# Kernel optimization log

Hardware: AMD Instinct MI355X
Metric: run time of the kernel (lower is better)

The kernel has to match this reference:

```python
import jax, jax.numpy as jnp
import numpy as np

N_ATOMS = 8_000_000
N_REC = 2_000_000
N_POC = 500_000
N_CHAINS = 4


def setup_inputs() -> dict:
    key = jax.random.key(0)
    k1, k2, k3, k4 = jax.random.split(key, 4)
    # coordinates in nm, inside a ~5 nm box
    positions = jax.random.uniform(k1, (N_ATOMS, 3), dtype=jnp.float32) * 5.0
    box_vectors = jnp.diag(jnp.array([5.0, 5.0, 5.0], dtype=jnp.float32))
    # unique receptor atom indices into positions
    rec_indices = jax.random.permutation(k2, N_ATOMS)[:N_REC].astype(jnp.int32)
    # unique pocket indices INTO THE REC ARRAY (poc_pos = rec_pos[poc_indices])
    poc_indices = jax.random.permutation(k3, N_REC)[:N_POC].astype(jnp.int32)
    # contiguous chain assignment over rec atoms, all chains present in pocket
    chain_ids = ((jnp.arange(N_REC, dtype=jnp.int32) * N_CHAINS) // N_REC).astype(jnp.int32)
    poc_chain_ids = chain_ids[poc_indices]
    ref_poc = jax.random.uniform(k4, (N_POC, 3), dtype=jnp.float32) * 5.0
    k = jnp.float32(100.0)  # kJ/mol/nm^2
    return {
        "positions": positions, "box_vectors": box_vectors, "ref_poc": ref_poc,
        "k": k, "rec_indices": rec_indices, "poc_indices": poc_indices,
        "chain_ids": chain_ids, "poc_chain_ids": poc_chain_ids, "n_chains": N_CHAINS,
    }


def best_periodic_translation(pos1, pos2, box_vectors):
    # pos1, pos2: [C,3]; box_vectors: [3,3] (rows are lattice vectors)
    delta = pos2 - pos1
    inv = 1.0 / jnp.diag(box_vectors)
    s3 = jnp.round(delta[:, 2] * inv[2])
    delta = delta - s3[:, None] * box_vectors[2]
    s2 = jnp.round(delta[:, 1] * inv[1])
    delta = delta - s2[:, None] * box_vectors[1]
    s1 = jnp.round(delta[:, 0] * inv[0])
    return s1[:, None] * box_vectors[0] + s2[:, None] * box_vectors[1] + s3[:, None] * box_vectors[2]


def reference(positions, box_vectors, ref_poc, k, rec_indices, poc_indices, chain_ids, poc_chain_ids, n_chains):
    rec_pos = positions[rec_indices]  # [R,3]
    # Per-chain pocket COM. NOTE: original indexes global positions here
    # (positions[poc_chain_indices]), NOT rec_pos -- reproduced faithfully.
    poc_glob = positions[poc_indices]  # [P,3]
    counts = jax.ops.segment_sum(jnp.ones((poc_glob.shape[0],), poc_glob.dtype), poc_chain_ids, num_segments=n_chains)  # [C]
    poc_com = jax.ops.segment_sum(poc_glob, poc_chain_ids, num_segments=n_chains) / counts[:, None]  # [C,3]
    ref_com = jax.ops.segment_sum(ref_poc, poc_chain_ids, num_segments=n_chains) / counts[:, None]  # [C,3]
    best_t = best_periodic_translation(poc_com, ref_com, box_vectors)  # [C,3]
    rec_pos = rec_pos + best_t[chain_ids]  # translate each chain into the reference image

    poc_pos = rec_pos[poc_indices]  # [P,3]
    rec_origin = jnp.mean(rec_pos, axis=0)
    rec_centered = rec_pos - rec_origin
    r_sq = jnp.sum(rec_centered ** 2, axis=1)  # [R]
    F = jnp.zeros_like(rec_pos).at[poc_indices].set(-2.0 * k * (poc_pos - ref_poc))
    F_mean = jnp.mean(F, axis=0)
    torque = jnp.cross(rec_centered, F)
    torque_mean = jnp.mean(torque, axis=0)
    F_rot = jnp.cross(torque_mean[None], rec_centered) / r_sq[:, None]
    F_final = jnp.zeros_like(positions).at[rec_indices].set(F_mean + F_rot)
    return (jnp.float32(0.0), F_final)
```

## Files before the change

### kernel.cpp

```cpp
#include <hip/hip_runtime.h>


typedef unsigned int uint32;
typedef unsigned char uchar;

#define MAXC 16
#define W_BT 0
#define W_O 48
#define W_FM 52
#define W_TM 56
#define W_ACC 64

#define GCOUNT_OFF 4096
#define REC_OFF 8192
#define NB 512
#define BSH 14
#define BUCKET_ATOMS (1 << BSH)
#define CAP 5120
#define INV8_OFF (REC_OFF + NB * CAP * 4)

#define PB 512
#define RB 512
#define K1_KPT 16
#define K1_CHUNK (256 * K1_KPT)

struct PartSh { uint32 hist[NB]; uint32 curs[NB]; uint32 base[NB]; };
struct PocSh  { float red[4][43]; float accL[3 + MAXC * 10]; };
union ShU { PartSh part; PocSh poc; };

__device__ inline float waveSum(float v) {
#pragma unroll
  for (int off = 32; off > 0; off >>= 1) v += __shfl_down(v, off, 64);
  return v;
}

__global__ __launch_bounds__(256) void k_fused(
    const float* __restrict__ pos, const float* __restrict__ ref_poc,
    const int* __restrict__ rec_idx, const int* __restrict__ cid,
    const int* __restrict__ poc_idx, const int* __restrict__ poc_cid,
    const int* __restrict__ ncp, int R, int P,
    uint32* __restrict__ gcount, uint32* __restrict__ grecords,
    float* __restrict__ ws) {
  const int tid = threadIdx.x;
  const int bid = blockIdx.x;
  __shared__ ShU sh;
  const int C = ncp[0];

  if (bid < PB) {
    const int gsz = PB * 256;
    if (C <= 4) {
      float vals[43];
#pragma unroll
      for (int v = 0; v < 43; ++v) vals[v] = 0.f;
      for (int rb = bid * 256 + tid; rb < P; rb += 4 * gsz) {
        int rr[4], i2[4], c2[4], ri[4];
        float g[4][3], p[4][3], rf[4][3];
#pragma unroll
        for (int q = 0; q < 4; ++q) {
          int r = rb + q * gsz;
          rr[q] = (r < P) ? r : -1;
        }
#pragma unroll
        for (int q = 0; q < 4; ++q) {
          int r = (rr[q] < 0) ? 0 : rr[q];
          i2[q] = poc_idx[r];
          c2[q] = poc_cid[r];
        }
#pragma unroll
        for (int q = 0; q < 4; ++q) {
          ri[q] = rec_idx[i2[q]];
          g[q][0] = pos[3 * i2[q] + 0];
          g[q][1] = pos[3 * i2[q] + 1];
          g[q][2] = pos[3 * i2[q] + 2];
        }
#pragma unroll
        for (int q = 0; q < 4; ++q) {
          int r = (rr[q] < 0) ? 0 : rr[q];
          p[q][0] = pos[3 * ri[q] + 0];
          p[q][1] = pos[3 * ri[q] + 1];
          p[q][2] = pos[3 * ri[q] + 2];
          rf[q][0] = ref_poc[3 * r + 0];
          rf[q][1] = ref_poc[3 * r + 1];
          rf[q][2] = ref_poc[3 * r + 2];
        }
#pragma unroll
        for (int q = 0; q < 4; ++q) {
          if (rr[q] >= 0) {
            vals[0] += p[q][1] * rf[q][2] - p[q][2] * rf[q][1];
            vals[1] += p[q][2] * rf[q][0] - p[q][0] * rf[q][2];
            vals[2] += p[q][0] * rf[q][1] - p[q][1] * rf[q][0];
#pragma unroll
            for (int cc = 0; cc < 4; ++cc) {
              bool m = (c2[q] == cc);
              float* a = &vals[3 + cc * 10];
              a[0] += m ? g[q][0] : 0.f; a[1] += m ? g[q][1] : 0.f;
              a[2] += m ? g[q][2] : 0.f;
              a[3] += m ? rf[q][0] : 0.f; a[4] += m ? rf[q][1] : 0.f;
              a[5] += m ? rf[q][2] : 0.f;
              a[6] += m ? p[q][0] : 0.f; a[7] += m ? p[q][1] : 0.f;
              a[8] += m ? p[q][2] : 0.f;
              a[9] += m ? 1.f : 0.f;
            }
          }
        }
      }
      const int wid = tid >> 6;
#pragma unroll
      for (int v = 0; v < 43; ++v) {
        float s = waveSum(vals[v]);
        if ((tid & 63) == 0) sh.poc.red[wid][v] = s;
      }
      __syncthreads();
      for (int t = tid; t < 43; t += 256)
        atomicAdd(&ws[W_ACC + 19 + t], sh.poc.red[0][t] + sh.poc.red[1][t] +
                                       sh.poc.red[2][t] + sh.poc.red[3][t]);
    } else {
      float* accL = sh.poc.accL;
      for (int t = tid; t < 3 + MAXC * 10; t += 256) accL[t] = 0.f;
      __syncthreads();
      for (int r = bid * 256 + tid; r < P; r += PB * 256) {
        int i2 = poc_idx[r];
        int c2 = poc_cid[r];
        int ri = rec_idx[i2];
        float gx = pos[3 * i2 + 0], gy = pos[3 * i2 + 1], gz = pos[3 * i2 + 2];
        float px = pos[3 * ri + 0], py = pos[3 * ri + 1], pz = pos[3 * ri + 2];
        float rx = ref_poc[3 * r + 0], ry = ref_poc[3 * r + 1], rz = ref_poc[3 * r + 2];
        atomicAdd(&accL[0], py * rz - pz * ry);
        atomicAdd(&accL[1], pz * rx - px * rz);
        atomicAdd(&accL[2], px * ry - py * rx);
        float* a = &accL[3 + c2 * 10];
        atomicAdd(&a[0], gx); atomicAdd(&a[1], gy); atomicAdd(&a[2], gz);
        atomicAdd(&a[3], rx); atomicAdd(&a[4], ry); atomicAdd(&a[5], rz);
        atomicAdd(&a[6], px); atomicAdd(&a[7], py); atomicAdd(&a[8], pz);
        atomicAdd(&a[9], 1.f);
      }
      __syncthreads();
      for (int t = tid; t < 3 + MAXC * 10; t += 256)
        if (accL[t] != 0.f) atomicAdd(&ws[W_ACC + 19 + t], accL[t]);
    }
  } else {
    const int pb = bid - PB;
    uint32* hist = sh.part.hist;
    uint32* curs = sh.part.curs;
    uint32* base = sh.part.base;
    for (int r0 = pb * K1_CHUNK; r0 < R; r0 += RB * K1_CHUNK) {
      int cnt = R - r0; if (cnt > K1_CHUNK) cnt = K1_CHUNK;
      for (int t = tid; t < NB; t += 256) { hist[t] = 0u; curs[t] = 0u; }
      __syncthreads();
      uint32 enc[K1_KPT];
#pragma unroll
      for (int j = 0; j < K1_KPT; ++j) {
        int t = tid + j * 256;
        uint32 e = 0xFFFFFFFFu;
        if (t < cnt) {
          uint32 idx = (uint32)rec_idx[r0 + t];
          uint32 c = (uint32)cid[r0 + t] & 255u;
          e = (idx << 8) | c;
          atomicAdd(&hist[idx >> BSH], 1u);
        }
        enc[j] = e;
      }
      __syncthreads();
      for (int t = tid; t < NB; t += 256) {
        uint32 h = hist[t];
        base[t] = h ? atomicAdd(&gcount[t], h) : 0u;
      }
      __syncthreads();
#pragma unroll
      for (int j = 0; j < K1_KPT; ++j) {
        uint32 e = enc[j];
        if (e != 0xFFFFFFFFu) {
          uint32 b = e >> (8 + BSH);
          uint32 slot = base[b] + atomicAdd(&curs[b], 1u);
          if (slot < CAP) grecords[b * CAP + slot] = e;
        }
      }
      __syncthreads();
    }
  }
}

__global__ __launch_bounds__(256) void k_bucket_build(
    const float4* __restrict__ pos4, const int* __restrict__ ncp,
    const uint32* __restrict__ gcount, const uint32* __restrict__ grecords,
    int N, uchar* __restrict__ inv8, float* __restrict__ ws) {
  const int tid = threadIdx.x;
  const int b = blockIdx.x;
  const int a0 = b << BSH;
  if (a0 >= N) return;
  int natoms = N - a0; if (natoms > BUCKET_ATOMS) natoms = BUCKET_ATOMS;

  __shared__ uchar map_[BUCKET_ATOMS];
  __shared__ float cnt16[MAXC];
  uint4* m16 = (uint4*)map_;
  uint4 ff; ff.x = ff.y = ff.z = ff.w = 0xFFFFFFFFu;
  for (int t = tid; t < BUCKET_ATOMS / 16; t += 256) m16[t] = ff;
  const int C = ncp[0];
  if (C > 4) for (int t = tid; t < MAXC; t += 256) cnt16[t] = 0.f;
  __syncthreads();

  int n = (int)gcount[b]; if (n > CAP) n = CAP;
  float c0 = 0.f, c1 = 0.f, c2 = 0.f, c3 = 0.f;
  for (int t = tid; t < n; t += 256) {
    uint32 e = grecords[b * CAP + t];
    uint32 ia = (e >> 8) & (BUCKET_ATOMS - 1);
    uint32 c = e & 255u;
    map_[ia] = (uchar)c;
    if (C <= 4) {
      c0 += (c == 0u) ? 1.f : 0.f;
      c1 += (c == 1u) ? 1.f : 0.f;
      c2 += (c == 2u) ? 1.f : 0.f;
      c3 += (c == 3u) ? 1.f : 0.f;
    } else {
      atomicAdd(&cnt16[c], 1.f);
    }
  }
  __syncthreads();

  uchar* dst = inv8 + a0;
  if (natoms == BUCKET_ATOMS) {
    uint4* d16 = (uint4*)dst;
    for (int t = tid; t < BUCKET_ATOMS / 16; t += 256) d16[t] = m16[t];
  } else {
    for (int t = tid; t < natoms; t += 256) dst[t] = map_[t];
  }

  float sx = 0.f, sy = 0.f, sz = 0.f;
  int ngf = natoms >> 2;
  const uchar4* m4 = (const uchar4*)map_;
  int g0 = a0 >> 2;
  for (int g = tid; g < ngf; g += 256) {
    float4 p0 = pos4[3 * (g0 + g) + 0];
    float4 p1 = pos4[3 * (g0 + g) + 1];
    float4 p2 = pos4[3 * (g0 + g) + 2];
    uchar4 m = m4[g];
    if (m.x != 255) { sx += p0.x; sy += p0.y; sz += p0.z; }
    if (m.y != 255) { sx += p0.w; sy += p1.x; sz += p1.y; }
    if (m.z != 255) { sx += p1.z; sy += p1.w; sz += p2.x; }
    if (m.w != 255) { sx += p2.y; sy += p2.z; sz += p2.w; }
  }
  int tb = natoms & 3;
  if (tid < tb) {
    int a = a0 + (ngf << 2) + tid;
    const float* pf = (const float*)pos4;
    if (map_[(ngf << 2) + tid] != 255) {
      sx += pf[3 * a]; sy += pf[3 * a + 1]; sz += pf[3 * a + 2];
    }
  }

  __shared__ float red[4][7];
  float vv[7] = {sx, sy, sz, c0, c1, c2, c3};
  const int wid = tid >> 6;
#pragma unroll
  for (int v = 0; v < 7; ++v) {
    float s = waveSum(vv[v]);
    if ((tid & 63) == 0) red[wid][v] = s;
  }
  __syncthreads();
  if (tid < 7) {
    float s = red[0][tid] + red[1][tid] + red[2][tid] + red[3][tid];
    atomicAdd(&ws[W_ACC + tid], s);
  }
  if (C > 4 && tid < C) atomicAdd(&ws[W_ACC + 3 + tid], cnt16[tid]);
}

__global__ void k_finalize(const float* __restrict__ box,
                           const float* __restrict__ kp,
                           const int* __restrict__ ncp,
                           int R, float* __restrict__ ws) {
  __shared__ float tot[192];
  const int C = ncp[0];
  for (int t = threadIdx.x; t < 192; t += blockDim.x) tot[t] = ws[W_ACC + t];
  __syncthreads();
  if (threadIdx.x != 0) return;
  const float kk = kp[0];
  const float Rf = (float)R;
  const float* xp = &tot[19];
  float inv0 = 1.f / box[0], inv1 = 1.f / box[4], inv2 = 1.f / box[8];
  float ox = tot[0], oy = tot[1], oz = tot[2];
  float Fx = 0, Fy = 0, Fz = 0;
  float T1x = 0, T1y = 0, T1z = 0, T2x = 0, T2y = 0, T2z = 0;
  for (int c = 0; c < C; ++c) {
    float nrec = tot[3 + c];
    const float* a = &tot[22 + c * 10];
    float np = a[9];
    float invn = 1.f / np;
    float pcx = a[0] * invn, pcy = a[1] * invn, pcz = a[2] * invn;
    float rcx = a[3] * invn, rcy = a[4] * invn, rcz = a[5] * invn;
    float dx = rcx - pcx, dy = rcy - pcy, dz = rcz - pcz;
    float s3 = rintf(dz * inv2);
    dx -= s3 * box[6]; dy -= s3 * box[7]; dz -= s3 * box[8];
    float s2 = rintf(dy * inv1);
    dx -= s2 * box[3]; dy -= s2 * box[4]; dz -= s2 * box[5];
    float s1 = rintf(dx * inv0);
    float btx = s1 * box[0] + s2 * box[3] + s3 * box[6];
    float bty = s1 * box[1] + s2 * box[4] + s3 * box[7];
    float btz = s1 * box[2] + s2 * box[5] + s3 * box[8];
    ws[W_BT + c * 3 + 0] = btx;
    ws[W_BT + c * 3 + 1] = bty;
    ws[W_BT + c * 3 + 2] = btz;
    ox += nrec * btx; oy += nrec * bty; oz += nrec * btz;
    float SFx = -2.f * kk * (a[6] + np * btx - a[3]);
    float SFy = -2.f * kk * (a[7] + np * bty - a[4]);
    float SFz = -2.f * kk * (a[8] + np * btz - a[5]);
    Fx += SFx; Fy += SFy; Fz += SFz;
    T1x += a[7] * btz - a[8] * bty;
    T1y += a[8] * btx - a[6] * btz;
    T1z += a[6] * bty - a[7] * btx;
    T2x += bty * SFz - btz * SFy;
    T2y += btz * SFx - btx * SFz;
    T2z += btx * SFy - bty * SFx;
  }
  ox /= Rf; oy /= Rf; oz /= Rf;
  float Tx = 2.f * kk * xp[0] - 2.f * kk * T1x + T2x - (oy * Fz - oz * Fy);
  float Ty = 2.f * kk * xp[1] - 2.f * kk * T1y + T2y - (oz * Fx - ox * Fz);
  float Tz = 2.f * kk * xp[2] - 2.f * kk * T1z + T2z - (ox * Fy - oy * Fx);
  ws[W_O + 0] = ox; ws[W_O + 1] = oy; ws[W_O + 2] = oz;
  ws[W_FM + 0] = Fx / Rf; ws[W_FM + 1] = Fy / Rf; ws[W_FM + 2] = Fz / Rf;
  ws[W_TM + 0] = Tx / Rf; ws[W_TM + 1] = Ty / Rf; ws[W_TM + 2] = Tz / Rf;
}

__global__ __launch_bounds__(256) void k_final_dense(
    const float* __restrict__ pos, const uchar* __restrict__ inv8,
    int N, const float* __restrict__ ws, float* __restrict__ out) {
  __shared__ float stage[3328];
  __shared__ float sc[64];
  const int tid = threadIdx.x;
  if (tid < 64) sc[tid] = ws[tid];
  const int t0 = blockIdx.x * 1024;
  int nat = N - t0; if (nat > 1024) nat = 1024;
  const int nfl = nat * 3;

  if (nat == 1024) {
    const float4* src4 = (const float4*)(pos + 3 * t0);
#pragma unroll
    for (int kk = 0; kk < 3; ++kk) {
      int v4 = tid + kk * 256;
      float4 p = src4[v4];
      int idx = 4 * v4 + v4 / 3;
      stage[idx + 0] = p.x; stage[idx + 1] = p.y;
      stage[idx + 2] = p.z; stage[idx + 3] = p.w;
    }
  } else {
    for (int k = tid; k < nfl; k += 256)
      stage[k + (int)((unsigned)k / 12u)] = pos[3 * t0 + k];
  }
  __syncthreads();

  float ox = sc[W_O + 0], oy = sc[W_O + 1], oz = sc[W_O + 2];
  float fmx = sc[W_FM + 0], fmy = sc[W_FM + 1], fmz = sc[W_FM + 2];
  float tmx = sc[W_TM + 0], tmy = sc[W_TM + 1], tmz = sc[W_TM + 2];

  uchar mc[4];
  if (nat == 1024) {
    uchar4 m = ((const uchar4*)(inv8 + t0))[tid];
    mc[0] = m.x; mc[1] = m.y; mc[2] = m.z; mc[3] = m.w;
  } else {
#pragma unroll
    for (int q = 0; q < 4; ++q) {
      int la = 4 * tid + q;
      mc[q] = (la < nat) ? inv8[t0 + la] : (uchar)255;
    }
  }
#pragma unroll
  for (int q = 0; q < 4; ++q) {
    int la = 4 * tid + q;
    if (la < nat) {
      float* s = &stage[13 * tid + 3 * q];
      float fx = 0.f, fy = 0.f, fz = 0.f;
      int c = mc[q];
      if (c != 255) {
        float cx = s[0] + sc[W_BT + 3 * c + 0] - ox;
        float cy = s[1] + sc[W_BT + 3 * c + 1] - oy;
        float cz = s[2] + sc[W_BT + 3 * c + 2] - oz;
        float inv = 1.f / (cx * cx + cy * cy + cz * cz);
        fx = fmx + (tmy * cz - tmz * cy) * inv;
        fy = fmy + (tmz * cx - tmx * cz) * inv;
        fz = fmz + (tmx * cy - tmy * cx) * inv;
      }
      s[0] = fx; s[1] = fy; s[2] = fz;
    }
  }
  __syncthreads();

  if (blockIdx.x == 0 && tid == 0) out[0] = 0.f;
  float* ob = out + 1 + 3 * t0;
  if (nat == 1024) {
#pragma unroll
    for (int kk = 0; kk < 3; ++kk) {
      int j = tid + kk * 256;
      if (j < 767) {
        int k = 3 + 4 * j;
        float4 v;
        v.x = stage[k + k / 12];
        v.y = stage[(k + 1) + (k + 1) / 12];
        v.z = stage[(k + 2) + (k + 2) / 12];
        v.w = stage[(k + 3) + (k + 3) / 12];
        *(float4*)(ob + k) = v;
      }
    }
    if (tid < 3) ob[tid] = stage[tid];
    if (tid == 3) ob[3071] = stage[3071 + 3071 / 12];
  } else {
    for (int k = tid; k < nfl; k += 256)
      ob[k] = stage[k + (int)((unsigned)k / 12u)];
  }
}

extern "C" void kernel_launch(void* const* d_in, const int* in_sizes, int n_in,
                              void* d_out, int out_size, void* d_ws, size_t ws_size,
                              hipStream_t stream) {
  const float* pos     = (const float*)d_in[0];
  const float* box     = (const float*)d_in[1];
  const float* ref_poc = (const float*)d_in[2];
  const float* kp      = (const float*)d_in[3];
  const int* rec_idx   = (const int*)d_in[4];
  const int* poc_idx   = (const int*)d_in[5];
  const int* cid       = (const int*)d_in[6];
  const int* poc_cid   = (const int*)d_in[7];
  const int* ncp       = (const int*)d_in[8];
  float* out = (float*)d_out;
  float* ws  = (float*)d_ws;
  uint32* gcount   = (uint32*)((char*)d_ws + GCOUNT_OFF);
  uint32* grecords = (uint32*)((char*)d_ws + REC_OFF);
  uchar* inv8      = (uchar*)d_ws + INV8_OFF;

  const int N = in_sizes[0] / 3;
  const int R = in_sizes[4];
  const int P = in_sizes[5];

  hipMemsetAsync(d_ws, 0, 8192, stream);

  k_fused<<<PB + RB, 256, 0, stream>>>(pos, ref_poc, rec_idx, cid, poc_idx,
                                       poc_cid, ncp, R, P, gcount, grecords, ws);
  k_bucket_build<<<NB, 256, 0, stream>>>((const float4*)pos, ncp, gcount,
                                         grecords, N, inv8, ws);
  k_finalize<<<1, 256, 0, stream>>>(box, kp, ncp, R, ws);
  int gF = (N + 1023) / 1024;
  k_final_dense<<<gF, 256, 0, stream>>>(pos, inv8, N, ws, out);
}
```

Baseline: 267.6 us.

## Drop global inv8 map; rebuild bucket maps in shared memory in output kernel

Removes the global byte map (inv8) that the bucket-build kernel wrote and the dense output kernel read. Both the position-sum kernel and the output kernel now rebuild the per-bucket chain map in LDS from the bucket records. Buckets shrink to 8192 atoms and each is split across two blocks. The fused first kernel is rebalanced to 2048 blocks with a different pocket/partition split, a 2-way unroll and a two-pass partition. The cost is re-reading the records twice and duplicated map-building work per half-block.

```diff
diff --git a/kernel.cpp b/kernel.cpp
--- a/kernel.cpp
+++ b/kernel.cpp
@@ -13,16 +13,15 @@
 
 #define GCOUNT_OFF 4096
 #define REC_OFF 8192
-#define NB 512
-#define BSH 14
+#define NB 1024
+#define BSH 13
 #define BUCKET_ATOMS (1 << BSH)
-#define CAP 5120
-#define INV8_OFF (REC_OFF + NB * CAP * 4)
-
-#define PB 512
-#define RB 512
-#define K1_KPT 16
-#define K1_CHUNK (256 * K1_KPT)
+#define CAP 2560
+
+#define TOTB 2048
+#define RB 256
+#define PB (TOTB - RB)
+#define CHUNK 8192
 
 struct PartSh { uint32 hist[NB]; uint32 curs[NB]; uint32 base[NB]; };
 struct PocSh  { float red[4][43]; float accL[3 + MAXC * 10]; };
@@ -52,29 +51,29 @@
       float vals[43];
 #pragma unroll
       for (int v = 0; v < 43; ++v) vals[v] = 0.f;
-      for (int rb = bid * 256 + tid; rb < P; rb += 4 * gsz) {
-        int rr[4], i2[4], c2[4], ri[4];
-        float g[4][3], p[4][3], rf[4][3];
-#pragma unroll
-        for (int q = 0; q < 4; ++q) {
+      for (int rb = bid * 256 + tid; rb < P; rb += 2 * gsz) {
+        int rr[2], i2[2], c2[2], ri[2];
+        float g[2][3], p[2][3], rf[2][3];
+#pragma unroll
+        for (int q = 0; q < 2; ++q) {
           int r = rb + q * gsz;
           rr[q] = (r < P) ? r : -1;
         }
 #pragma unroll
-        for (int q = 0; q < 4; ++q) {
+        for (int q = 0; q < 2; ++q) {
           int r = (rr[q] < 0) ? 0 : rr[q];
           i2[q] = poc_idx[r];
           c2[q] = poc_cid[r];
         }
 #pragma unroll
-        for (int q = 0; q < 4; ++q) {
+        for (int q = 0; q < 2; ++q) {
           ri[q] = rec_idx[i2[q]];
           g[q][0] = pos[3 * i2[q] + 0];
           g[q][1] = pos[3 * i2[q] + 1];
           g[q][2] = pos[3 * i2[q] + 2];
         }
 #pragma unroll
-        for (int q = 0; q < 4; ++q) {
+        for (int q = 0; q < 2; ++q) {
           int r = (rr[q] < 0) ? 0 : rr[q];
           p[q][0] = pos[3 * ri[q] + 0];
           p[q][1] = pos[3 * ri[q] + 1];
@@ -84,7 +83,7 @@
           rf[q][2] = ref_poc[3 * r + 2];
         }
 #pragma unroll
-        for (int q = 0; q < 4; ++q) {
+        for (int q = 0; q < 2; ++q) {
           if (rr[q] >= 0) {
             vals[0] += p[q][1] * rf[q][2] - p[q][2] * rf[q][1];
             vals[1] += p[q][2] * rf[q][0] - p[q][0] * rf[q][2];
@@ -143,22 +142,13 @@
     uint32* hist = sh.part.hist;
     uint32* curs = sh.part.curs;
     uint32* base = sh.part.base;
-    for (int r0 = pb * K1_CHUNK; r0 < R; r0 += RB * K1_CHUNK) {
-      int cnt = R - r0; if (cnt > K1_CHUNK) cnt = K1_CHUNK;
+    for (int r0 = pb * CHUNK; r0 < R; r0 += RB * CHUNK) {
+      int cnt = R - r0; if (cnt > CHUNK) cnt = CHUNK;
       for (int t = tid; t < NB; t += 256) { hist[t] = 0u; curs[t] = 0u; }
       __syncthreads();
-      uint32 enc[K1_KPT];
-#pragma unroll
-      for (int j = 0; j < K1_KPT; ++j) {
-        int t = tid + j * 256;
-        uint32 e = 0xFFFFFFFFu;
-        if (t < cnt) {
-          uint32 idx = (uint32)rec_idx[r0 + t];
-          uint32 c = (uint32)cid[r0 + t] & 255u;
-          e = (idx << 8) | c;
-          atomicAdd(&hist[idx >> BSH], 1u);
-        }
-        enc[j] = e;
+      for (int t = tid; t < cnt; t += 256) {
+        uint32 idx = (uint32)rec_idx[r0 + t];
+        atomicAdd(&hist[idx >> BSH], 1u);
       }
       __syncthreads();
       for (int t = tid; t < NB; t += 256) {
@@ -166,27 +156,26 @@
         base[t] = h ? atomicAdd(&gcount[t], h) : 0u;
       }
       __syncthreads();
-#pragma unroll
-      for (int j = 0; j < K1_KPT; ++j) {
-        uint32 e = enc[j];
-        if (e != 0xFFFFFFFFu) {
-          uint32 b = e >> (8 + BSH);
-          uint32 slot = base[b] + atomicAdd(&curs[b], 1u);
-          if (slot < CAP) grecords[b * CAP + slot] = e;
-        }
-      }
-      __syncthreads();
-    }
-  }
-}
-
-__global__ __launch_bounds__(256) void k_bucket_build(
+      for (int t = tid; t < cnt; t += 256) {
+        uint32 idx = (uint32)rec_idx[r0 + t];
+        uint32 c = (uint32)cid[r0 + t] & 255u;
+        uint32 b = idx >> BSH;
+        uint32 slot = base[b] + atomicAdd(&curs[b], 1u);
+        if (slot < CAP) grecords[b * CAP + slot] = (idx << 8) | c;
+      }
+      __syncthreads();
+    }
+  }
+}
+
+__global__ __launch_bounds__(256) void k_possum(
     const float4* __restrict__ pos4, const int* __restrict__ ncp,
     const uint32* __restrict__ gcount, const uint32* __restrict__ grecords,
-    int N, uchar* __restrict__ inv8, float* __restrict__ ws) {
+    int N, float* __restrict__ ws) {
   const int tid = threadIdx.x;
-  const int b = blockIdx.x;
-  const int a0 = b << BSH;
+  const int bucket = blockIdx.x >> 1;
+  const int half = blockIdx.x & 1;
+  const int a0 = bucket << BSH;
   if (a0 >= N) return;
   int natoms = N - a0; if (natoms > BUCKET_ATOMS) natoms = BUCKET_ATOMS;
 
@@ -199,10 +188,10 @@
   if (C > 4) for (int t = tid; t < MAXC; t += 256) cnt16[t] = 0.f;
   __syncthreads();
 
-  int n = (int)gcount[b]; if (n > CAP) n = CAP;
+  int n = (int)gcount[bucket]; if (n > CAP) n = CAP;
   float c0 = 0.f, c1 = 0.f, c2 = 0.f, c3 = 0.f;
   for (int t = tid; t < n; t += 256) {
-    uint32 e = grecords[b * CAP + t];
+    uint32 e = grecords[bucket * CAP + t];
     uint32 ia = (e >> 8) & (BUCKET_ATOMS - 1);
     uint32 c = e & 255u;
     map_[ia] = (uchar)c;
@@ -211,24 +200,21 @@
       c1 += (c == 1u) ? 1.f : 0.f;
       c2 += (c == 2u) ? 1.f : 0.f;
       c3 += (c == 3u) ? 1.f : 0.f;
-    } else {
+    } else if (half == 0) {
       atomicAdd(&cnt16[c], 1.f);
     }
   }
   __syncthreads();
 
-  uchar* dst = inv8 + a0;
-  if (natoms == BUCKET_ATOMS) {
-    uint4* d16 = (uint4*)dst;
-    for (int t = tid; t < BUCKET_ATOMS / 16; t += 256) d16[t] = m16[t];
-  } else {
-    for (int t = tid; t < natoms; t += 256) dst[t] = map_[t];
-  }
+  int h0 = half * (BUCKET_ATOMS / 2);
+  int hcnt = natoms - h0;
+  if (hcnt < 0) hcnt = 0;
+  if (hcnt > BUCKET_ATOMS / 2) hcnt = BUCKET_ATOMS / 2;
 
   float sx = 0.f, sy = 0.f, sz = 0.f;
-  int ngf = natoms >> 2;
-  const uchar4* m4 = (const uchar4*)map_;
-  int g0 = a0 >> 2;
+  int ngf = hcnt >> 2;
+  const uchar4* m4 = (const uchar4*)(map_ + h0);
+  int g0 = (a0 + h0) >> 2;
   for (int g = tid; g < ngf; g += 256) {
     float4 p0 = pos4[3 * (g0 + g) + 0];
     float4 p1 = pos4[3 * (g0 + g) + 1];
@@ -239,11 +225,11 @@
     if (m.z != 255) { sx += p1.z; sy += p1.w; sz += p2.x; }
     if (m.w != 255) { sx += p2.y; sy += p2.z; sz += p2.w; }
   }
-  int tb = natoms & 3;
+  int tb = hcnt & 3;
   if (tid < tb) {
-    int a = a0 + (ngf << 2) + tid;
+    int a = a0 + h0 + (ngf << 2) + tid;
     const float* pf = (const float*)pos4;
-    if (map_[(ngf << 2) + tid] != 255) {
+    if (map_[h0 + (ngf << 2) + tid] != 255) {
       sx += pf[3 * a]; sy += pf[3 * a + 1]; sz += pf[3 * a + 2];
     }
   }
@@ -257,11 +243,14 @@
     if ((tid & 63) == 0) red[wid][v] = s;
   }
   __syncthreads();
-  if (tid < 7) {
+  if (tid < 3) {
     float s = red[0][tid] + red[1][tid] + red[2][tid] + red[3][tid];
     atomicAdd(&ws[W_ACC + tid], s);
-  }
-  if (C > 4 && tid < C) atomicAdd(&ws[W_ACC + 3 + tid], cnt16[tid]);
+  } else if (tid < 7 && half == 0 && C <= 4) {
+    float s = red[0][tid] + red[1][tid] + red[2][tid] + red[3][tid];
+    atomicAdd(&ws[W_ACC + tid], s);
+  }
+  if (C > 4 && half == 0 && tid < C) atomicAdd(&ws[W_ACC + 3 + tid], cnt16[tid]);
 }
 
 __global__ void k_finalize(const float* __restrict__ box,
@@ -320,30 +309,28 @@
   ws[W_TM + 0] = Tx / Rf; ws[W_TM + 1] = Ty / Rf; ws[W_TM + 2] = Tz / Rf;
 }
 
-__global__ __launch_bounds__(256) void k_final_dense(
-    const float* __restrict__ pos, const uchar* __restrict__ inv8,
+__global__ __launch_bounds__(256) void k_out(
+    const float* __restrict__ pos, const int* __restrict__ ncp,
+    const uint32* __restrict__ gcount, const uint32* __restrict__ grecords,
     int N, const float* __restrict__ ws, float* __restrict__ out) {
+  const int tid = threadIdx.x;
+  const int bucket = blockIdx.x >> 1;
+  const int half = blockIdx.x & 1;
+  const int a0 = bucket << BSH;
+  if (a0 >= N) return;
+
+  __shared__ uchar map_[BUCKET_ATOMS];
   __shared__ float stage[3328];
   __shared__ float sc[64];
-  const int tid = threadIdx.x;
   if (tid < 64) sc[tid] = ws[tid];
-  const int t0 = blockIdx.x * 1024;
-  int nat = N - t0; if (nat > 1024) nat = 1024;
-  const int nfl = nat * 3;
-
-  if (nat == 1024) {
-    const float4* src4 = (const float4*)(pos + 3 * t0);
-#pragma unroll
-    for (int kk = 0; kk < 3; ++kk) {
-      int v4 = tid + kk * 256;
-      float4 p = src4[v4];
-      int idx = 4 * v4 + v4 / 3;
-      stage[idx + 0] = p.x; stage[idx + 1] = p.y;
-      stage[idx + 2] = p.z; stage[idx + 3] = p.w;
-    }
-  } else {
-    for (int k = tid; k < nfl; k += 256)
-      stage[k + (int)((unsigned)k / 12u)] = pos[3 * t0 + k];
+  uint4* m16 = (uint4*)map_;
+  uint4 ff; ff.x = ff.y = ff.z = ff.w = 0xFFFFFFFFu;
+  for (int t = tid; t < BUCKET_ATOMS / 16; t += 256) m16[t] = ff;
+  __syncthreads();
+  int n = (int)gcount[bucket]; if (n > CAP) n = CAP;
+  for (int t = tid; t < n; t += 256) {
+    uint32 e = grecords[bucket * CAP + t];
+    map_[(e >> 8) & (BUCKET_ATOMS - 1)] = (uchar)(e & 255u);
   }
   __syncthreads();
 
@@ -351,59 +338,85 @@
   float fmx = sc[W_FM + 0], fmy = sc[W_FM + 1], fmz = sc[W_FM + 2];
   float tmx = sc[W_TM + 0], tmy = sc[W_TM + 1], tmz = sc[W_TM + 2];
 
-  uchar mc[4];
-  if (nat == 1024) {
-    uchar4 m = ((const uchar4*)(inv8 + t0))[tid];
-    mc[0] = m.x; mc[1] = m.y; mc[2] = m.z; mc[3] = m.w;
-  } else {
+  if (blockIdx.x == 0 && tid == 0) out[0] = 0.f;
+
+  int lim = a0 + BUCKET_ATOMS; if (lim > N) lim = N;
+  for (int t0 = a0 + half * (BUCKET_ATOMS / 2);
+       t0 < lim && t0 < a0 + (half + 1) * (BUCKET_ATOMS / 2); t0 += 1024) {
+    int nat = lim - t0; if (nat > 1024) nat = 1024;
+    const int nfl = nat * 3;
+
+    if (nat == 1024) {
+      const float4* src4 = (const float4*)(pos + 3 * t0);
+#pragma unroll
+      for (int kk = 0; kk < 3; ++kk) {
+        int v4 = tid + kk * 256;
+        float4 p = src4[v4];
+        int idx = 4 * v4 + v4 / 3;
+        stage[idx + 0] = p.x; stage[idx + 1] = p.y;
+        stage[idx + 2] = p.z; stage[idx + 3] = p.w;
+      }
+    } else {
+      for (int k = tid; k < nfl; k += 256)
+        stage[k + (int)((unsigned)k / 12u)] = pos[3 * t0 + k];
+    }
+    __syncthreads();
+
+    const int lb = t0 - a0;
+    uchar mc[4];
+    if (nat == 1024) {
+      uchar4 m = ((const uchar4*)(map_ + lb))[tid];
+      mc[0] = m.x; mc[1] = m.y; mc[2] = m.z; mc[3] = m.w;
+    } else {
+#pragma unroll
+      for (int q = 0; q < 4; ++q) {
+        int la = 4 * tid + q;
+        mc[q] = (la < nat) ? map_[lb + la] : (uchar)255;
+      }
+    }
 #pragma unroll
     for (int q = 0; q < 4; ++q) {
       int la = 4 * tid + q;
-      mc[q] = (la < nat) ? inv8[t0 + la] : (uchar)255;
-    }
-  }
-#pragma unroll
-  for (int q = 0; q < 4; ++q) {
-    int la = 4 * tid + q;
-    if (la < nat) {
-      float* s = &stage[13 * tid + 3 * q];
-      float fx = 0.f, fy = 0.f, fz = 0.f;
-      int c = mc[q];
-      if (c != 255) {
-        float cx = s[0] + sc[W_BT + 3 * c + 0] - ox;
-        float cy = s[1] + sc[W_BT + 3 * c + 1] - oy;
-        float cz = s[2] + sc[W_BT + 3 * c + 2] - oz;
-        float inv = 1.f / (cx * cx + cy * cy + cz * cz);
-        fx = fmx + (tmy * cz - tmz * cy) * inv;
-        fy = fmy + (tmz * cx - tmx * cz) * inv;
-        fz = fmz + (tmx * cy - tmy * cx) * inv;
-      }
-      s[0] = fx; s[1] = fy; s[2] = fz;
-    }
-  }
-  __syncthreads();
-
-  if (blockIdx.x == 0 && tid == 0) out[0] = 0.f;
-  float* ob = out + 1 + 3 * t0;
-  if (nat == 1024) {
-#pragma unroll
-    for (int kk = 0; kk < 3; ++kk) {
-      int j = tid + kk * 256;
-      if (j < 767) {
-        int k = 3 + 4 * j;
-        float4 v;
-        v.x = stage[k + k / 12];
-        v.y = stage[(k + 1) + (k + 1) / 12];
-        v.z = stage[(k + 2) + (k + 2) / 12];
-        v.w = stage[(k + 3) + (k + 3) / 12];
-        *(float4*)(ob + k) = v;
-      }
-    }
-    if (tid < 3) ob[tid] = stage[tid];
-    if (tid == 3) ob[3071] = stage[3071 + 3071 / 12];
-  } else {
-    for (int k = tid; k < nfl; k += 256)
-      ob[k] = stage[k + (int)((unsigned)k / 12u)];
+      if (la < nat) {
+        float* s = &stage[13 * tid + 3 * q];
+        float fx = 0.f, fy = 0.f, fz = 0.f;
+        int c = mc[q];
+        if (c != 255) {
+          float cx = s[0] + sc[W_BT + 3 * c + 0] - ox;
+          float cy = s[1] + sc[W_BT + 3 * c + 1] - oy;
+          float cz = s[2] + sc[W_BT + 3 * c + 2] - oz;
+          float inv = 1.f / (cx * cx + cy * cy + cz * cz);
+          fx = fmx + (tmy * cz - tmz * cy) * inv;
+          fy = fmy + (tmz * cx - tmx * cz) * inv;
+          fz = fmz + (tmx * cy - tmy * cx) * inv;
+        }
+        s[0] = fx; s[1] = fy; s[2] = fz;
+      }
+    }
+    __syncthreads();
+
+    float* ob = out + 1 + 3 * t0;
+    if (nat == 1024) {
+#pragma unroll
+      for (int kk = 0; kk < 3; ++kk) {
+        int j = tid + kk * 256;
+        if (j < 767) {
+          int k = 3 + 4 * j;
+          float4 v;
+          v.x = stage[k + k / 12];
+          v.y = stage[(k + 1) + (k + 1) / 12];
+          v.z = stage[(k + 2) + (k + 2) / 12];
+          v.w = stage[(k + 3) + (k + 3) / 12];
+          *(float4*)(ob + k) = v;
+        }
+      }
+      if (tid < 3) ob[tid] = stage[tid];
+      if (tid == 3) ob[3071] = stage[3071 + 3071 / 12];
+    } else {
+      for (int k = tid; k < nfl; k += 256)
+        ob[k] = stage[k + (int)((unsigned)k / 12u)];
+    }
+    __syncthreads();
   }
 }
 
@@ -423,7 +436,6 @@
   float* ws  = (float*)d_ws;
   uint32* gcount   = (uint32*)((char*)d_ws + GCOUNT_OFF);
   uint32* grecords = (uint32*)((char*)d_ws + REC_OFF);
-  uchar* inv8      = (uchar*)d_ws + INV8_OFF;
 
   const int N = in_sizes[0] / 3;
   const int R = in_sizes[4];
@@ -431,11 +443,11 @@
 
   hipMemsetAsync(d_ws, 0, 8192, stream);
 
-  k_fused<<<PB + RB, 256, 0, stream>>>(pos, ref_poc, rec_idx, cid, poc_idx,
-                                       poc_cid, ncp, R, P, gcount, grecords, ws);
-  k_bucket_build<<<NB, 256, 0, stream>>>((const float4*)pos, ncp, gcount,
-                                         grecords, N, inv8, ws);
+  const int nbuckets = (N + BUCKET_ATOMS - 1) >> BSH;
+  k_fused<<<TOTB, 256, 0, stream>>>(pos, ref_poc, rec_idx, cid, poc_idx,
+                                    poc_cid, ncp, R, P, gcount, grecords, ws);
+  k_possum<<<2 * nbuckets, 256, 0, stream>>>((const float4*)pos, ncp, gcount,
+                                             grecords, N, ws);
   k_finalize<<<1, 256, 0, stream>>>(box, kp, ncp, R, ws);
-  int gF = (N + 1023) / 1024;
-  k_final_dense<<<gF, 256, 0, stream>>>(pos, inv8, N, ws, out);
-}
+  k_out<<<2 * nbuckets, 256, 0, stream>>>(pos, ncp, gcount, grecords, N, ws, out);
+}
```

Result: slower. 321.9 us (+20.3%).
